# Kernel tuning notes

Hardware: AMD Instinct MI355X
Metric: run time of the kernel (lower is better)

Reference implementation:

```python
import jax, jax.numpy as jnp
import numpy as np


def setup_inputs() -> dict:
    key = jax.random.key(0)
    k1, k2 = jax.random.split(key)
    B, H, W, E = 8, 32, 32, 256   # latent grid (NHWC layout, as in vector_quantize)
    N_E = 16384                   # codebook size
    x = jax.random.normal(k1, (B, H, W, E), dtype=jnp.float32)
    codebook = jax.random.normal(k2, (N_E, E), dtype=jnp.float32)
    return {"x": x, "codebook": codebook}


def reference(x, codebook):
    # d[b,h,w,k] = ||x[b,h,w] - codebook[k]||^2 (expanded form, as in source)
    x_sq = jnp.sum(x * x, axis=-1, keepdims=True)            # [B,H,W,1]
    cb_sq = jnp.sum(codebook * codebook, axis=1)              # [N_E]
    cross = jnp.einsum('bhwe,ke->bhwk', x, codebook)          # [B,H,W,N_E]
    d = x_sq + cb_sq - 2.0 * cross
    indices = jnp.argmin(d, axis=-1)                          # [B,H,W]
    x_q = jnp.take(codebook, indices, axis=0)                 # one-hot @ codebook == row gather
    # straight-through / ReplaceGrad: forward value is x_q, gradient flows to x
    return x + jax.lax.stop_gradient(x_q - x)
```

## Files before the change

kernel.cpp:

```cpp
#include <hip/hip_runtime.h>
#include <stdint.h>

#define M_PIX 8192
#define N_CB  16384
#define KD    256

typedef float f32x4 __attribute__((ext_vector_type(4)));
typedef long long ll2 __attribute__((ext_vector_type(2)));
typedef unsigned long long ull;

#define OFF_CF8  (0ULL)
#define OFF_XF8  (4ULL << 20)
#define OFF_CBSQ (6ULL << 20)
#define OFF_SLOT (7ULL << 20)
#define WS_REQ   (15ULL << 20)

__device__ __forceinline__ unsigned int fkey(float s) {
  unsigned int f = __float_as_uint(s);
  return f ^ ((unsigned int)(((int)f) >> 31) | 0x80000000u);
}
__device__ __forceinline__ unsigned char f2e4m3(float v) {
  float av = fminf(fabsf(v), 448.0f);
  const unsigned s = (__float_as_uint(v) >> 24) & 0x80u;
  unsigned m;
  if (av >= 0.015625f) {
    unsigned u = __float_as_uint(av);
    u += 0x7FFFFu + ((u >> 20) & 1u);
    m = (((u >> 23) - 120u) << 3) | ((u >> 20) & 7u);
  } else {
    m = (unsigned)(int)rintf(av * 512.0f);
  }
  return (unsigned char)(s | m);
}
__device__ __forceinline__ void gl_lds16(const unsigned char* g, char* l) {
  __builtin_amdgcn_global_load_lds(
      (const __attribute__((address_space(1))) unsigned int*)(const void*)g,
      (__attribute__((address_space(3))) unsigned int*)(void*)l,
      16, 0, 0);
}
__device__ __forceinline__ void ins2f(float k, float& v1, float& v2) {
  v2 = fminf(v2, fmaxf(v1, k));
  v1 = fminf(v1, k);
}

__global__ __launch_bounds__(256) void prep_kernel(
    const float* __restrict__ x, const float* __restrict__ cb,
    unsigned char* __restrict__ Cf8, unsigned char* __restrict__ Xf8,
    float* __restrict__ cbsq) {
  const int wid = threadIdx.x >> 6, lane = threadIdx.x & 63;
  const int row = blockIdx.x * 4 + wid;
  const bool isCb = (row < N_CB);
  const int rowL = isCb ? row : row - N_CB;
  const float* src = (isCb ? cb : x) + (size_t)rowL * KD;
  const float4 v = ((const float4*)src)[lane];
  const int k0 = lane * 4;
  const int p0 = (k0 & 0x87) | ((k0 & 0x18) << 2) | ((k0 >> 2) & 0x18);
  uchar4 pk;
  pk.x = f2e4m3(v.x); pk.y = f2e4m3(v.y); pk.z = f2e4m3(v.z); pk.w = f2e4m3(v.w);
  *(uchar4*)(void*)((isCb ? Cf8 : Xf8) + (size_t)rowL * KD + p0) = pk;
  if (isCb) {
    float ss = v.x*v.x + v.y*v.y + v.z*v.z + v.w*v.w;
    #pragma unroll
    for (int off = 32; off > 0; off >>= 1) ss += __shfl_xor(ss, off);
    if (lane == 0) cbsq[rowL] = ss;
  }
}


__global__ __launch_bounds__(256, 4) void gemm_top2_kernel(
    const unsigned char* __restrict__ Xf8, const unsigned char* __restrict__ Cf8,
    const float* __restrict__ cbsq, float2* __restrict__ slots) {
  __shared__ __align__(16) char smem[36864];
  char* A_s = smem;
  char* B_s = smem + 16384;
  float* v1p = (float*)smem;
  float* v2p = (float*)(smem + 18432);

  const int tid = threadIdx.x;
  const int wid = tid >> 6, lane = tid & 63;
  const int wy = wid >> 1, wx = wid & 1;
  const int q = lane >> 4, c = lane & 15;

  const int bx = blockIdx.x & 7, bg = blockIdx.x >> 3;
  const int mt = bg >> 4;
  const int nt = bx * 16 + (bg & 15);
  const int m0 = mt * 128, n0 = nt * 128;

  int abase[4], bbase[4];
  #pragma unroll
  for (int i = 0; i < 4; i++) {
    abase[i] = (wy * 64 + i * 16 + c) * 128 + q * 32;
    bbase[i] = (wx * 64 + i * 16 + c) * 128 + q * 32;
  }

  const f32x4 zf = {0.f, 0.f, 0.f, 0.f};
  f32x4 acc[4][4];
  #pragma unroll
  for (int i = 0; i < 4; i++)
    #pragma unroll
    for (int j = 0; j < 4; j++) acc[i][j] = zf;

  #pragma unroll
  for (int hk = 0; hk < 2; hk++) {
    if (hk) __syncthreads();
    #pragma unroll
    for (int j = 0; j < 4; j++) {
      const int chunk = j * 4 + wid;
      const int row = chunk * 8 + (lane >> 3);
      const int gb = (lane & 7) * 16 + hk * 128;
      gl_lds16(Xf8 + (size_t)(m0 + row) * KD + gb, A_s + chunk * 1024);
      gl_lds16(Cf8 + (size_t)(n0 + row) * KD + gb, B_s + chunk * 1024);
    }
    __syncthreads();
    #pragma unroll
    for (int kp = 0; kp < 2; kp++) {
      ll2 bfr[4];
      #pragma unroll
      for (int ni = 0; ni < 4; ni++)
        bfr[ni] = *(const ll2*)(const void*)(B_s + bbase[ni] + kp * 16);
      #pragma unroll
      for (int mi = 0; mi < 4; mi++) {
        const ll2 af = *(const ll2*)(const void*)(A_s + abase[mi] + kp * 16);
        #pragma unroll
        for (int ni = 0; ni < 4; ni++) {
          acc[mi][ni] = __builtin_amdgcn_mfma_f32_16x16x32_fp8_fp8(af.x, bfr[ni].x, acc[mi][ni], 0, 0, 0);
          acc[mi][ni] = __builtin_amdgcn_mfma_f32_16x16x32_fp8_fp8(af.y, bfr[ni].y, acc[mi][ni], 0, 0, 0);
        }
      }
    }
  }
  __syncthreads();

  float cs[4]; unsigned colp[4];
  #pragma unroll
  for (int ni = 0; ni < 4; ni++) {
    colp[ni] = wx * 64 + ni * 16 + c;
    cs[ni] = cbsq[n0 + colp[ni]];
  }
  const float FINF = __uint_as_float(0x7F800000u);

  #pragma unroll
  for (int mi = 0; mi < 4; mi++) {
    #pragma unroll
    for (int r = 0; r < 4; r++) {
      float v1 = FINF, v2 = FINF;
      #pragma unroll
      for (int ni = 0; ni < 4; ni++) {
        const float s = fmaf(-2.f, acc[mi][ni][r], cs[ni]);
        ins2f(__uint_as_float((__float_as_uint(s) & 0xFFFFFF80u) | colp[ni]),
              v1, v2);
      }
      const int row = wy * 64 + mi * 16 + q * 4 + r;
      const int slot = wx * 16 + c;
      v1p[row * 36 + slot] = v1;
      v2p[row * 36 + slot] = v2;
    }
  }
  __syncthreads();

  {
    const int srow = tid >> 1, half = tid & 1;
    float v1 = FINF, v2 = FINF;
    #pragma unroll
    for (int jj = 0; jj < 2; jj++) {
      const float4 a = *(const float4*)(const void*)(v1p + srow * 36 + half * 16 + jj * 8);
      const float4 a2 = *(const float4*)(const void*)(v1p + srow * 36 + half * 16 + jj * 8 + 4);
      const float4 b = *(const float4*)(const void*)(v2p + srow * 36 + half * 16 + jj * 8);
      const float4 b2 = *(const float4*)(const void*)(v2p + srow * 36 + half * 16 + jj * 8 + 4);
      ins2f(a.x, v1, v2);  ins2f(a.y, v1, v2);
      ins2f(a.z, v1, v2);  ins2f(a.w, v1, v2);
      ins2f(a2.x, v1, v2); ins2f(a2.y, v1, v2);
      ins2f(a2.z, v1, v2); ins2f(a2.w, v1, v2);
      ins2f(b.x, v1, v2);  ins2f(b.y, v1, v2);
      ins2f(b.z, v1, v2);  ins2f(b.w, v1, v2);
      ins2f(b2.x, v1, v2); ins2f(b2.y, v1, v2);
      ins2f(b2.z, v1, v2); ins2f(b2.w, v1, v2);
    }
    const float b1 = __shfl_xor(v1, 1), b2 = __shfl_xor(v2, 1);
    const float hi = fmaxf(v1, b1);
    v1 = fminf(v1, b1);
    v2 = fminf(fminf(v2, b2), hi);
    if (!half)
      slots[(size_t)nt * M_PIX + m0 + srow] = make_float2(v1, v2);
  }
}

__global__ __launch_bounds__(256) void reduce_rescore_gather(
    const float* __restrict__ x, const float* __restrict__ cb,
    const float* __restrict__ cbsq, const float2* __restrict__ slots,
    float* __restrict__ out) {
  const int wid = threadIdx.x >> 6, lane = threadIdx.x & 63;
  const int pixel = blockIdx.x * 4 + wid;

  const float2 sA = slots[(size_t)lane * M_PIX + pixel];
  const float2 sB = slots[(size_t)(64 + lane) * M_PIX + pixel];
  const float sc[4] = {sA.x, sA.y, sB.x, sB.y};
  float mn = fminf(fminf(sc[0], sc[1]), fminf(sc[2], sc[3]));
  #pragma unroll
  for (int off = 1; off < 64; off <<= 1) mn = fminf(mn, __shfl_xor(mn, off));
  const float thr = mn + 10.0f;

  const float4 xv = ((const float4*)x)[(size_t)pixel * 64 + lane];
  ull best = ~0ULL;
  #pragma unroll
  for (int j = 0; j < 4; j++) {
    ull mask = __ballot(sc[j] < thr);
    while (mask) {
      const int src = (int)__ffsll((long long)mask) - 1;
      mask &= mask - 1;
      const float val = __shfl(sc[j], src);
      const unsigned ij = (unsigned)(((j >> 1) * 64 + src) * 128) +
                          (__float_as_uint(val) & 127u);
      const float4 cv = ((const float4*)cb)[(size_t)ij * 64 + lane];
      float d = xv.x*cv.x + xv.y*cv.y + xv.z*cv.z + xv.w*cv.w;
      #pragma unroll
      for (int off = 1; off < 64; off <<= 1) d += __shfl_xor(d, off);
      const float sv = fmaf(-2.f, d, cbsq[ij]);
      const ull k = ((ull)fkey(sv) << 32) | ij;
      best = k < best ? k : best;
    }
  }
  const unsigned w = (unsigned)best;
  ((float4*)out)[(size_t)pixel * 64 + lane] = ((const float4*)cb)[(size_t)w * 64 + lane];
}

__global__ __launch_bounds__(256) void fallback_kernel(
    const float* __restrict__ x, const float* __restrict__ cb,
    float* __restrict__ out) {
  __shared__ float xs[256];
  __shared__ unsigned long long keys[4];
  __shared__ int widx;
  const int p = blockIdx.x;
  const int tid = threadIdx.x, wid = tid >> 6, lane = tid & 63;
  xs[tid] = x[(size_t)p * KD + tid];
  __syncthreads();
  const float4 xv = ((const float4*)xs)[lane];
  float bestS = 3.4e38f; int bestI = 0;
  for (int k = wid; k < N_CB; k += 4) {
    const float4 cv = ((const float4*)cb)[(size_t)k * 64 + lane];
    float t = cv.x*(cv.x - 2.f*xv.x) + cv.y*(cv.y - 2.f*xv.y)
            + cv.z*(cv.z - 2.f*xv.z) + cv.w*(cv.w - 2.f*xv.w);
    #pragma unroll
    for (int off = 1; off < 64; off <<= 1) t += __shfl_xor(t, off);
    if (t < bestS) { bestS = t; bestI = k; }
  }
  if (lane == 0)
    keys[wid] = ((unsigned long long)fkey(bestS) << 32) | (unsigned int)bestI;
  __syncthreads();
  if (tid == 0) {
    unsigned long long m = keys[0];
    for (int i = 1; i < 4; i++) if (keys[i] < m) m = keys[i];
    widx = (int)(unsigned int)(m & 0xFFFFFFFFULL);
  }
  __syncthreads();
  out[(size_t)p * KD + tid] = cb[(size_t)widx * KD + tid];
}

extern "C" void kernel_launch(void* const* d_in, const int* in_sizes, int n_in,
                              void* d_out, int out_size, void* d_ws, size_t ws_size,
                              hipStream_t stream) {
  const float* x  = (const float*)d_in[0];
  const float* cb = (const float*)d_in[1];
  float* out = (float*)d_out;

  if (ws_size < WS_REQ) {
    fallback_kernel<<<M_PIX, 256, 0, stream>>>(x, cb, out);
    return;
  }

  char* ws = (char*)d_ws;
  unsigned char* Cf8 = (unsigned char*)(ws + OFF_CF8);
  unsigned char* Xf8 = (unsigned char*)(ws + OFF_XF8);
  float* cbsq        = (float*)(ws + OFF_CBSQ);
  float2* slots      = (float2*)(ws + OFF_SLOT);

  prep_kernel<<<(N_CB + M_PIX) / 4, 256, 0, stream>>>(x, cb, Cf8, Xf8, cbsq);
  gemm_top2_kernel<<<M_PIX, 256, 0, stream>>>(Xf8, Cf8, cbsq, slots);
  reduce_rescore_gather<<<M_PIX / 4, 256, 0, stream>>>(x, cb, cbsq, slots, out);
}
```

Before: 155.2 us.

## Use gfx950 scaled 16x16x128 FP8 MFMA with XOR-swizzled LDS layout

Replaces pairs of 16x16x32 FP8 MFMAs with the CDNA4 scaled 16x16x128 f8f6f4 MFMA, using unit scales (0x7F). This cuts the instruction count and lets each lane load 32 contiguous bytes. The prep kernel's K-permutation is dropped, so FP8 rows are now stored in natural order. LDS tiles are XOR-swizzled on both the async global-to-LDS load side and the read side to avoid bank conflicts. The occupancy hint drops from 4 to 3 waves per SIMD to allow more registers for the wider operands.

```diff
diff --git a/kernel.cpp b/kernel.cpp
--- a/kernel.cpp
+++ b/kernel.cpp
@@ -6,7 +6,8 @@
 #define KD    256
 
 typedef float f32x4 __attribute__((ext_vector_type(4)));
-typedef long long ll2 __attribute__((ext_vector_type(2)));
+typedef int   i32x4 __attribute__((ext_vector_type(4)));
+typedef int   i32x8 __attribute__((ext_vector_type(8)));
 typedef unsigned long long ull;
 
 #define OFF_CF8  (0ULL)
@@ -42,6 +43,11 @@
   v2 = fminf(v2, fmaxf(v1, k));
   v1 = fminf(v1, k);
 }
+__device__ __forceinline__ i32x8 ld32(const char* p, int addr) {
+  const i32x4 lo = *(const i32x4*)(const void*)(p + addr);
+  const i32x4 hi = *(const i32x4*)(const void*)(p + (addr ^ 16));
+  return (i32x8){lo.x, lo.y, lo.z, lo.w, hi.x, hi.y, hi.z, hi.w};
+}
 
 __global__ __launch_bounds__(256) void prep_kernel(
     const float* __restrict__ x, const float* __restrict__ cb,
@@ -53,11 +59,9 @@
   const int rowL = isCb ? row : row - N_CB;
   const float* src = (isCb ? cb : x) + (size_t)rowL * KD;
   const float4 v = ((const float4*)src)[lane];
-  const int k0 = lane * 4;
-  const int p0 = (k0 & 0x87) | ((k0 & 0x18) << 2) | ((k0 >> 2) & 0x18);
   uchar4 pk;
   pk.x = f2e4m3(v.x); pk.y = f2e4m3(v.y); pk.z = f2e4m3(v.z); pk.w = f2e4m3(v.w);
-  *(uchar4*)(void*)((isCb ? Cf8 : Xf8) + (size_t)rowL * KD + p0) = pk;
+  *(uchar4*)(void*)((isCb ? Cf8 : Xf8) + (size_t)rowL * KD + lane * 4) = pk;
   if (isCb) {
     float ss = v.x*v.x + v.y*v.y + v.z*v.z + v.w*v.w;
     #pragma unroll
@@ -67,7 +71,7 @@
 }
 
 
-__global__ __launch_bounds__(256, 4) void gemm_top2_kernel(
+__global__ __launch_bounds__(256, 3) void gemm_top2_kernel(
     const unsigned char* __restrict__ Xf8, const unsigned char* __restrict__ Cf8,
     const float* __restrict__ cbsq, float2* __restrict__ slots) {
   __shared__ __align__(16) char smem[36864];
@@ -86,11 +90,12 @@
   const int nt = bx * 16 + (bg & 15);
   const int m0 = mt * 128, n0 = nt * 128;
 
-  int abase[4], bbase[4];
+  const int swz = (c & 7) << 4;
+  int aaddr[4], baddr[4];
   #pragma unroll
   for (int i = 0; i < 4; i++) {
-    abase[i] = (wy * 64 + i * 16 + c) * 128 + q * 32;
-    bbase[i] = (wx * 64 + i * 16 + c) * 128 + q * 32;
+    aaddr[i] = (((wy * 64 + i * 16 + c) * 128) + q * 32) ^ swz;
+    baddr[i] = (((wx * 64 + i * 16 + c) * 128) + q * 32) ^ swz;
   }
 
   const f32x4 zf = {0.f, 0.f, 0.f, 0.f};
@@ -100,33 +105,34 @@
     #pragma unroll
     for (int j = 0; j < 4; j++) acc[i][j] = zf;
 
+  const int srow8 = lane >> 3;
+  const int sgb = ((lane & 7) ^ srow8) * 16;
+
   #pragma unroll
   for (int hk = 0; hk < 2; hk++) {
     if (hk) __syncthreads();
     #pragma unroll
     for (int j = 0; j < 4; j++) {
       const int chunk = j * 4 + wid;
-      const int row = chunk * 8 + (lane >> 3);
-      const int gb = (lane & 7) * 16 + hk * 128;
+      const int row = chunk * 8 + srow8;
+      const int gb = sgb + hk * 128;
       gl_lds16(Xf8 + (size_t)(m0 + row) * KD + gb, A_s + chunk * 1024);
       gl_lds16(Cf8 + (size_t)(n0 + row) * KD + gb, B_s + chunk * 1024);
     }
     __syncthreads();
-    #pragma unroll
-    for (int kp = 0; kp < 2; kp++) {
-      ll2 bfr[4];
+    i32x8 bfr[4];
+    #pragma unroll
+    for (int ni = 0; ni < 4; ni++)
+      bfr[ni] = ld32(B_s, baddr[ni]);
+    #pragma unroll
+    for (int mi = 0; mi < 4; mi++) {
+      const i32x8 af = ld32(A_s, aaddr[mi]);
       #pragma unroll
       for (int ni = 0; ni < 4; ni++)
-        bfr[ni] = *(const ll2*)(const void*)(B_s + bbase[ni] + kp * 16);
-      #pragma unroll
-      for (int mi = 0; mi < 4; mi++) {
-        const ll2 af = *(const ll2*)(const void*)(A_s + abase[mi] + kp * 16);
-        #pragma unroll
-        for (int ni = 0; ni < 4; ni++) {
-          acc[mi][ni] = __builtin_amdgcn_mfma_f32_16x16x32_fp8_fp8(af.x, bfr[ni].x, acc[mi][ni], 0, 0, 0);
-          acc[mi][ni] = __builtin_amdgcn_mfma_f32_16x16x32_fp8_fp8(af.y, bfr[ni].y, acc[mi][ni], 0, 0, 0);
-        }
-      }
+        acc[mi][ni] = __builtin_amdgcn_mfma_scale_f32_16x16x128_f8f6f4(
+            af, bfr[ni], acc[mi][ni], 0, 0,
+            0, 0x7F7F7F7F,
+            0, 0x7F7F7F7F);
     }
   }
   __syncthreads();
```

Measured after the change: 144.9 us. -6.7%, faster.
